# Performance work log

Measured on AMD Instinct MI355X. Metric: run time of the kernel, lower is better.

## Reference

```python
import jax, jax.numpy as jnp
import numpy as np

K = 121          # kernel_size
C = 3            # channels
PAD = (K - 1) // 2  # 60, replicate padding so output matches input spatial size


def setup_inputs() -> dict:
    key = jax.random.key(0)
    k1, k2 = jax.random.split(key)
    x = jax.random.normal(k1, (8, C, 512, 512), dtype=jnp.float32)
    sigma = jax.random.uniform(k2, (), dtype=jnp.float32)
    return {"x": x, "sigma": sigma}


def _gaussian_kernel(sigma):
    # sigma -> sigma*8 + 16, variance = sigma**2 (as in torch forward)
    s = sigma * 8.0 + 16.0
    variance = s * s
    coord = jnp.arange(K, dtype=jnp.float32) - (K - 1) / 2.0  # centered coords
    diff = -(coord[:, None] ** 2 + coord[None, :] ** 2)       # [K,K], -((x-m)^2+(y-m)^2)
    kern = jnp.exp(diff / (2.0 * variance))
    # the 1/(2*pi*variance) prefactor cancels under normalization
    kern = kern / jnp.sum(kern)
    return kern


def reference(x, sigma):
    kern = _gaussian_kernel(sigma)
    # depthwise weights: [out_ch=C, in_ch/groups=1, K, K]
    w = jnp.broadcast_to(kern[None, None, :, :], (C, 1, K, K))
    # replicate padding (torch 'replicate' == jnp 'edge')
    xp = jnp.pad(x, ((0, 0), (0, 0), (PAD, PAD), (PAD, PAD)), mode="edge")
    out = jax.lax.conv_general_dilated(
        xp, w,
        window_strides=(1, 1),
        padding="VALID",
        dimension_numbers=("NCHW", "OIHW", "NCHW"),
        feature_group_count=C,
    )
    return out
```

## Files before the change

### kernel.cpp

```cpp
#include <hip/hip_runtime.h>


#define HH    512
#define WW    512
#define PLANE (512 * 512)
#define NIMG  24
#define ROWF  672

__global__ void wk_prep(const float* __restrict__ sigma,
                        float* __restrict__ wg) {
    const int tid = threadIdx.x;
    const float s = sigma[0] * 8.0f + 16.0f;
    const float inv2v = 1.0f / (2.0f * s * s);
    float sum = 0.0f;
    #pragma unroll
    for (int k = 0; k <= 120; ++k) {
        const float c = (float)k - 60.0f;
        sum += __expf(-c * c * inv2v);
    }
    float g = 0.0f;
    if (tid < 121) {
        const float c = (float)tid - 60.0f;
        g = __expf(-c * c * inv2v);
    }
    wg[tid] = g / sum;
}

__device__ __forceinline__ int swz_off(int col) {
    const int u = col >> 2;
    return ((u ^ ((u >> 3) & 7)) << 2) + (col & 3);
}

#define V_OCT_P(A, B, C, KO)                                              \
    { _Pragma("unroll")                                                   \
      for (int ki = 0; ki < 8; ++ki) {                                    \
          int rr = r0 - 44 + (KO) * 8 + ki;                               \
          rr = rr < 0 ? 0 : (rr > HH - 1 ? HH - 1 : rr);                  \
          C[ki] = *(const float2*)&src[(size_t)rr * WW];                  \
      }                                                                   \
      *(float4*)&wq[0] = *(const float4*)&wg[(KO) * 8];                   \
      *(float4*)&wq[4] = *(const float4*)&wg[(KO) * 8 + 4];               \
      _Pragma("unroll")                                                   \
      for (int ki = 0; ki < 8; ++ki) {                                    \
          const float wk = wq[ki];                                        \
          _Pragma("unroll")                                               \
          for (int j = 0; j < 8; ++j) {                                   \
              const int idx = ki + j;                                     \
              const float2 v = (idx < 8) ? A[idx] : B[idx - 8];           \
              vac[j].x += wk * v.x; vac[j].y += wk * v.y;                 \
          }                                                               \
      }                                                                   \
    }

#define V_OCT_NP(A, B, KO)                                                \
    { *(float4*)&wq[0] = *(const float4*)&wg[(KO) * 8];                   \
      *(float4*)&wq[4] = *(const float4*)&wg[(KO) * 8 + 4];               \
      _Pragma("unroll")                                                   \
      for (int ki = 0; ki < 8; ++ki) {                                    \
          const float wk = wq[ki];                                        \
          _Pragma("unroll")                                               \
          for (int j = 0; j < 8; ++j) {                                   \
              const int idx = ki + j;                                     \
              const float2 v = (idx < 8) ? A[idx] : B[idx - 8];           \
              vac[j].x += wk * v.x; vac[j].y += wk * v.y;                 \
          }                                                               \
      }                                                                   \
    }

#define LOADG2(DA, DB, G)                                                 \
    { const int u_  = 2 * (G);                                            \
      const int o1_ = (((u_ ^ ((u_ >> 3) & 7)) << 2)) ^ parx4;            \
      const int o2_ = o1_ ^ 4;                                            \
      *(float4*)&DA[0] = *(const float4*)(bs + o1_);                      \
      *(float4*)&DA[4] = *(const float4*)(bs + o2_);                      \
      *(float4*)&DB[0] = *(const float4*)(bs + o1_ + 256);                \
      *(float4*)&DB[4] = *(const float4*)(bs + o2_ + 256); }

#define H_OCT2(A0, A1, A2, A3, B0, B1, B2, B3, KO)                        \
    { LOADG2(A3, B3, L + (KO) + 3)                                        \
      *(float4*)&wq[0] = *(const float4*)&wg[(KO) * 8];                   \
      *(float4*)&wq[4] = *(const float4*)&wg[(KO) * 8 + 4];               \
      _Pragma("unroll")                                                   \
      for (int ki = 0; ki < 8; ++ki) {                                    \
          const float wk = wq[ki];                                        \
          _Pragma("unroll")                                               \
          for (int j = 0; j < 8; ++j) {                                   \
              const int idx = ki + j;                                     \
              const float vA = (idx < 8) ? A0[idx]                        \
                             : (idx < 16) ? A1[idx - 8] : A2[idx - 16];   \
              const float vB = (idx < 8) ? B0[idx]                        \
                             : (idx < 16) ? B1[idx - 8] : B2[idx - 16];   \
              accA[j] += wk * vA;                                         \
              accB[j] += wk * vB;                                         \
          }                                                               \
      }                                                                   \
    }

__global__ __launch_bounds__(256, 6) void blur_fused(
        const float* __restrict__ x, const float* __restrict__ wg,
        float* __restrict__ out) {
    __shared__ float sm[8 * ROWF];
    const int tid = threadIdx.x;

    const int lid   = blockIdx.x + gridDim.x * blockIdx.y;
    const int tile  = (lid & 7) * 192 + (lid >> 3);
    const int r0    = (tile & 63) * 8;
    const int plane = tile >> 6;

    const int c0 = tid * 2;
    const float* __restrict__ src = x + (size_t)plane * PLANE + c0;

    float2 w0[8], w1[8], w2[8], vac[8];
    float  wq[8];
    #pragma unroll
    for (int m = 0; m < 8; ++m) {
        int rr = r0 - 60 + m;
        rr = rr < 0 ? 0 : rr;
        w0[m] = *(const float2*)&src[(size_t)rr * WW];
    }
    #pragma unroll
    for (int m = 0; m < 8; ++m) {
        int rr = r0 - 52 + m;
        rr = rr < 0 ? 0 : rr;
        w1[m] = *(const float2*)&src[(size_t)rr * WW];
    }
    #pragma unroll
    for (int j = 0; j < 8; ++j) vac[j] = make_float2(0.f, 0.f);

    #pragma unroll 1
    for (int ko = 0; ko < 15; ko += 3) {
        V_OCT_P(w0, w1, w2, ko)
        V_OCT_P(w1, w2, w0, ko + 1)
        V_OCT_P(w2, w0, w1, ko + 2)
    }
    V_OCT_NP(w0, w1, 15)

    {
        const int off = swz_off(c0 + 60);
        #pragma unroll
        for (int j = 0; j < 8; ++j)
            *(float2*)&sm[j * ROWF + (off ^ ((j & 1) << 2))] = vac[j];
    }
    __syncthreads();

    if (tid < 36) {
        const int p = (tid < 15) ? tid * 4
                    : (tid < 34) ? 572 + (tid - 15) * 4
                                 : 648 + (tid - 34) * 4;
        const int u    = p >> 2;
        const int off0 = (u ^ ((u >> 3) & 7)) << 2;
        const int sof0 = (tid < 15) ? swz_off(60) : swz_off(571);
        #pragma unroll
        for (int r8 = 0; r8 < 8; ++r8) {
            const int pp = (r8 & 1) << 2;
            const float v = (tid < 34) ? sm[r8 * ROWF + (sof0 ^ pp)] : 0.0f;
            *(float4*)&sm[r8 * ROWF + (off0 ^ pp)] = make_float4(v, v, v, v);
        }
    }
    __syncthreads();

    const int r = tid >> 5;
    const int L = tid & 31;
    const int parx4 = (r & 1) << 2;
    const float* __restrict__ bs = sm + r * ROWF;

    float a0[8], a1[8], a2[8], a3[8];
    float b0[8], b1[8], b2[8], b3[8];
    float accA[8], accB[8];
    #pragma unroll
    for (int j = 0; j < 8; ++j) { accA[j] = 0.0f; accB[j] = 0.0f; }

    LOADG2(a0, b0, L)
    LOADG2(a1, b1, L + 1)
    LOADG2(a2, b2, L + 2)

    #pragma unroll 1
    for (int ko = 0; ko < 16; ko += 4) {
        H_OCT2(a0, a1, a2, a3, b0, b1, b2, b3, ko)
        H_OCT2(a1, a2, a3, a0, b1, b2, b3, b0, ko + 1)
        H_OCT2(a2, a3, a0, a1, b2, b3, b0, b1, ko + 2)
        H_OCT2(a3, a0, a1, a2, b3, b0, b1, b2, ko + 3)
    }

    float* __restrict__ dst = out + (size_t)plane * PLANE
                                  + (size_t)(r0 + r) * WW + L * 8;
    *(float4*)(dst)       = make_float4(accA[0], accA[1], accA[2], accA[3]);
    *(float4*)(dst + 4)   = make_float4(accA[4], accA[5], accA[6], accA[7]);
    *(float4*)(dst + 256) = make_float4(accB[0], accB[1], accB[2], accB[3]);
    *(float4*)(dst + 260) = make_float4(accB[4], accB[5], accB[6], accB[7]);
}

extern "C" void kernel_launch(void* const* d_in, const int* in_sizes, int n_in,
                              void* d_out, int out_size, void* d_ws, size_t ws_size,
                              hipStream_t stream) {
    const float* x     = (const float*)d_in[0];
    const float* sigma = (const float*)d_in[1];
    float* out = (float*)d_out;
    float* wg  = (float*)d_ws;
    wk_prep<<<dim3(1), dim3(128), 0, stream>>>(sigma, wg);
    blur_fused<<<dim3(HH / 8, NIMG), dim3(256), 0, stream>>>(x, wg, out);
}
```

Baseline: 114.7 us.

## Use packed fp16 dot2 for horizontal Gaussian pass

```diff
diff --git a/kernel.cpp b/kernel.cpp
--- a/kernel.cpp
+++ b/kernel.cpp
@@ -6,6 +6,37 @@
 #define PLANE (512 * 512)
 #define NIMG  24
 #define ROWF  672
+
+typedef __fp16 h2 __attribute__((ext_vector_type(2)));
+
+__device__ __forceinline__ h2 u2h(unsigned u) {
+    union { unsigned u; h2 h; } x; x.u = u; return x.h;
+}
+__device__ __forceinline__ unsigned h2u(h2 h) {
+    union { unsigned u; h2 h; } x; x.h = h; return x.u;
+}
+
+#if __has_builtin(__builtin_amdgcn_cvt_pkrtz)
+#define PKRTZ(a, b) __builtin_amdgcn_cvt_pkrtz((a), (b))
+#else
+__device__ __forceinline__ h2 PKRTZ(float a, float b) {
+    h2 r; r[0] = (__fp16)a; r[1] = (__fp16)b; return r;
+}
+#endif
+
+#if __has_builtin(__builtin_amdgcn_alignbit)
+#define ALNB(hi, lo) __builtin_amdgcn_alignbit((hi), (lo), 16)
+#else
+#define ALNB(hi, lo) ((((unsigned)(lo)) >> 16) | (((unsigned)(hi)) << 16))
+#endif
+
+__device__ __forceinline__ float fdot2f(h2 a, h2 b, float c) {
+#if __has_builtin(__builtin_amdgcn_fdot2)
+    return __builtin_amdgcn_fdot2(a, b, c, false);
+#else
+    return (float)a[0] * (float)b[0] + (float)a[1] * (float)b[1] + c;
+#endif
+}
 
 __global__ void wk_prep(const float* __restrict__ sigma,
                         float* __restrict__ wg) {
@@ -24,6 +55,13 @@
         g = __expf(-c * c * inv2v);
     }
     wg[tid] = g / sum;
+    if (tid < 64) {
+        const float c0 = (float)(2 * tid) - 60.0f;
+        const float c1 = (float)(2 * tid + 1) - 60.0f;
+        const float w0 = (2 * tid     <= 120) ? __expf(-c0 * c0 * inv2v) / sum : 0.0f;
+        const float w1 = (2 * tid + 1 <= 120) ? __expf(-c1 * c1 * inv2v) / sum : 0.0f;
+        ((unsigned*)(wg + 128))[tid] = h2u(PKRTZ(w0, w1));
+    }
 }
 
 __device__ __forceinline__ int swz_off(int col) {
@@ -67,31 +105,43 @@
       }                                                                   \
     }
 
-#define LOADG2(DA, DB, G)                                                 \
+#define LOADG2H(DA, DB, G)                                                \
     { const int u_  = 2 * (G);                                            \
       const int o1_ = (((u_ ^ ((u_ >> 3) & 7)) << 2)) ^ parx4;            \
       const int o2_ = o1_ ^ 4;                                            \
-      *(float4*)&DA[0] = *(const float4*)(bs + o1_);                      \
-      *(float4*)&DA[4] = *(const float4*)(bs + o2_);                      \
-      *(float4*)&DB[0] = *(const float4*)(bs + o1_ + 256);                \
-      *(float4*)&DB[4] = *(const float4*)(bs + o2_ + 256); }
-
-#define H_OCT2(A0, A1, A2, A3, B0, B1, B2, B3, KO)                        \
-    { LOADG2(A3, B3, L + (KO) + 3)                                        \
-      *(float4*)&wq[0] = *(const float4*)&wg[(KO) * 8];                   \
-      *(float4*)&wq[4] = *(const float4*)&wg[(KO) * 8 + 4];               \
-      _Pragma("unroll")                                                   \
-      for (int ki = 0; ki < 8; ++ki) {                                    \
-          const float wk = wq[ki];                                        \
+      const float4 qa0 = *(const float4*)(bs + o1_);                      \
+      const float4 qa1 = *(const float4*)(bs + o2_);                      \
+      const float4 qb0 = *(const float4*)(bs + o1_ + 256);                \
+      const float4 qb1 = *(const float4*)(bs + o2_ + 256);                \
+      DA[0] = PKRTZ(qa0.x, qa0.y); DA[1] = PKRTZ(qa0.z, qa0.w);           \
+      DA[2] = PKRTZ(qa1.x, qa1.y); DA[3] = PKRTZ(qa1.z, qa1.w);           \
+      DB[0] = PKRTZ(qb0.x, qb0.y); DB[1] = PKRTZ(qb0.z, qb0.w);           \
+      DB[2] = PKRTZ(qb1.x, qb1.y); DB[3] = PKRTZ(qb1.z, qb1.w); }
+
+#define H_OCTD(A0, A1, A3, B0, B1, B3, KO)                                \
+    { LOADG2H(A3, B3, L + (KO) + 3)                                       \
+      const unsigned WA[8] = {h2u(A0[0]), h2u(A0[1]), h2u(A0[2]),         \
+                              h2u(A0[3]), h2u(A1[0]), h2u(A1[1]),         \
+                              h2u(A1[2]), h2u(A1[3])};                    \
+      const unsigned WB[8] = {h2u(B0[0]), h2u(B0[1]), h2u(B0[2]),         \
+                              h2u(B0[3]), h2u(B1[0]), h2u(B1[1]),         \
+                              h2u(B1[2]), h2u(B1[3])};                    \
+      unsigned SA[7], SB[7];                                              \
+      _Pragma("unroll")                                                   \
+      for (int d = 0; d < 7; ++d) {                                       \
+          SA[d] = ALNB(WA[d + 1], WA[d]);                                 \
+          SB[d] = ALNB(WB[d + 1], WB[d]);                                 \
+      }                                                                   \
+      _Pragma("unroll")                                                   \
+      for (int t = 0; t < 4; ++t) {                                       \
+          const h2 wp = u2h(wgu[(KO) * 4 + t]);                           \
           _Pragma("unroll")                                               \
           for (int j = 0; j < 8; ++j) {                                   \
-              const int idx = ki + j;                                     \
-              const float vA = (idx < 8) ? A0[idx]                        \
-                             : (idx < 16) ? A1[idx - 8] : A2[idx - 16];   \
-              const float vB = (idx < 8) ? B0[idx]                        \
-                             : (idx < 16) ? B1[idx - 8] : B2[idx - 16];   \
-              accA[j] += wk * vA;                                         \
-              accB[j] += wk * vB;                                         \
+              const int d = t + (j >> 1);                                 \
+              const h2 vA = (j & 1) ? u2h(SA[d]) : u2h(WA[d]);            \
+              const h2 vB = (j & 1) ? u2h(SB[d]) : u2h(WB[d]);            \
+              accA[j] = fdot2f(wp, vA, accA[j]);                          \
+              accB[j] = fdot2f(wp, vB, accB[j]);                          \
           }                                                               \
       }                                                                   \
     }
@@ -163,23 +213,24 @@
     const int L = tid & 31;
     const int parx4 = (r & 1) << 2;
     const float* __restrict__ bs = sm + r * ROWF;
-
-    float a0[8], a1[8], a2[8], a3[8];
-    float b0[8], b1[8], b2[8], b3[8];
+    const unsigned* __restrict__ wgu = (const unsigned*)(wg + 128);
+
+    h2 a0[4], a1[4], a2[4], a3[4];
+    h2 b0[4], b1[4], b2[4], b3[4];
     float accA[8], accB[8];
     #pragma unroll
     for (int j = 0; j < 8; ++j) { accA[j] = 0.0f; accB[j] = 0.0f; }
 
-    LOADG2(a0, b0, L)
-    LOADG2(a1, b1, L + 1)
-    LOADG2(a2, b2, L + 2)
+    LOADG2H(a0, b0, L)
+    LOADG2H(a1, b1, L + 1)
+    LOADG2H(a2, b2, L + 2)
 
     #pragma unroll 1
     for (int ko = 0; ko < 16; ko += 4) {
-        H_OCT2(a0, a1, a2, a3, b0, b1, b2, b3, ko)
-        H_OCT2(a1, a2, a3, a0, b1, b2, b3, b0, ko + 1)
-        H_OCT2(a2, a3, a0, a1, b2, b3, b0, b1, ko + 2)
-        H_OCT2(a3, a0, a1, a2, b3, b0, b1, b2, ko + 3)
+        H_OCTD(a0, a1, a3, b0, b1, b3, ko)
+        H_OCTD(a1, a2, a0, b1, b2, b0, ko + 1)
+        H_OCTD(a2, a3, a1, b2, b3, b1, ko + 2)
+        H_OCTD(a3, a0, a2, b3, b0, b2, ko + 3)
     }
 
     float* __restrict__ dst = out + (size_t)plane * PLANE
```

Result: slower. 128.3 us (+11.8%).
